# Performance work log

Measured on AMD Instinct MI355X. Metric: run time of the kernel, lower is better.

## Reference

```python
import jax, jax.numpy as jnp
import numpy as np

N = 50000        # nodes
E = 800000       # edges
IN_DIM, HID, OUT = 512, 256, 128
EPS = 1e-5       # PyG LayerNorm eps (added to std)


def setup_inputs() -> dict:
    key = jax.random.key(0)
    ks = jax.random.split(key, 24)
    def lin(k, i, o, scale=0.05):
        kw, kb = jax.random.split(k)
        return (jax.random.normal(kw, (i, o), jnp.float32) * scale,
                jax.random.normal(kb, (o,), jnp.float32) * scale)
    x = jax.random.normal(ks[0], (N, IN_DIM), jnp.float32)
    edge_index = jax.random.randint(ks[1], (2, E), 0, N, jnp.int64)
    Wq1, bq1 = lin(ks[2], IN_DIM, HID)
    Wk1, bk1 = lin(ks[3], IN_DIM, HID)
    Wv1, bv1 = lin(ks[4], IN_DIM, HID)
    Ws1, bs1 = lin(ks[5], IN_DIM, HID)
    g1 = jnp.ones((HID,), jnp.float32)
    be1 = jnp.zeros((HID,), jnp.float32)
    Wq2, bq2 = lin(ks[6], HID, OUT)
    Wk2, bk2 = lin(ks[7], HID, OUT)
    Wv2, bv2 = lin(ks[8], HID, OUT)
    Ws2, bs2 = lin(ks[9], HID, OUT)
    g2 = jnp.ones((OUT,), jnp.float32)
    be2 = jnp.zeros((OUT,), jnp.float32)
    return dict(x=x, Wq1=Wq1, bq1=bq1, Wk1=Wk1, bk1=bk1, Wv1=Wv1, bv1=bv1,
                Ws1=Ws1, bs1=bs1, g1=g1, be1=be1,
                Wq2=Wq2, bq2=bq2, Wk2=Wk2, bk2=bk2, Wv2=Wv2, bv2=bv2,
                Ws2=Ws2, bs2=bs2, g2=g2, be2=be2, edge_index=edge_index)


def transformer_conv(x, edge_index, Wq, bq, Wk, bk, Wv, bv, Ws, bs):
    # PyG TransformerConv, heads=1, concat=True, root_weight=True
    src, dst = edge_index[0], edge_index[1]
    n = x.shape[0]
    d = Wq.shape[1]
    q = x @ Wq + bq                               # [N, d]
    k = x @ Wk + bk
    v = x @ Wv + bv
    score = (q[dst] * k[src]).sum(-1) / jnp.sqrt(jnp.asarray(d, x.dtype))  # [E]
    m = jax.ops.segment_max(score, dst, num_segments=n)     # per-target max
    e = jnp.exp(score - m[dst])
    denom = jax.ops.segment_sum(e, dst, num_segments=n)
    alpha = e / denom[dst]                         # scatter-softmax over in-edges
    agg = jax.ops.segment_sum(alpha[:, None] * v[src], dst, num_segments=n)
    return agg + (x @ Ws + bs)                     # root/skip connection


def graph_layer_norm(h, w, b):
    # PyG LayerNorm mode='graph', no batch: normalize over ALL entries
    h = h - h.mean()
    return h / (h.std() + EPS) * w + b


def reference(x, Wq1, bq1, Wk1, bk1, Wv1, bv1, Ws1, bs1, g1, be1,
              Wq2, bq2, Wk2, bk2, Wv2, bv2, Ws2, bs2, g2, be2, edge_index):
    a1 = graph_layer_norm(
        transformer_conv(x, edge_index, Wq1, bq1, Wk1, bk1, Wv1, bv1, Ws1, bs1),
        g1, be1)
    h1 = jax.nn.elu(a1)  # ELU(alpha=1.0)
    h2 = graph_layer_norm(
        transformer_conv(h1, edge_index, Wq2, bq2, Wk2, bk2, Wv2, bv2, Ws2, bs2),
        g2, be2)
    return h2
```

## Files before the change

kernel.cpp:

```cpp
#include <hip/hip_runtime.h>
#include <stdint.h>
#include <math.h>

#define IN_DIM 512
#define HID    256
#define OUTD   128
#define LN_EPS 1e-5f
#define NSLOT  2048

typedef unsigned short u16;
typedef unsigned int   u32;
typedef short short8 __attribute__((ext_vector_type(8)));
typedef float f32x4  __attribute__((ext_vector_type(4)));

__device__ __forceinline__ float bf2f(u32 h) {
  union { u32 u; float f; } c; c.u = h << 16; return c.f;
}
__device__ __forceinline__ u16 f2bf(float f) {
  union { float f; u32 u; } c; c.f = f;
  u32 u = c.u;
  return (u16)((u + 0x7FFFu + ((u >> 16) & 1u)) >> 16);
}

__device__ __forceinline__ void gload_lds16(const void* g, void* l) {
  __builtin_amdgcn_global_load_lds((const __attribute__((address_space(1))) void*)g,
                                   (__attribute__((address_space(3))) void*)l, 16, 0, 0);
}

__global__ __launch_bounds__(256) void k_prep(
    const float* __restrict__ x, u16* __restrict__ x_bf, int n4,
    const int* __restrict__ edst, int* __restrict__ deg, int E,
    const float* __restrict__ bq1, const float* __restrict__ bk1,
    const float* __restrict__ bv1, const float* __restrict__ bs1,
    const float* __restrict__ bq2, const float* __restrict__ bk2,
    const float* __restrict__ bv2, const float* __restrict__ bs2,
    float* __restrict__ bc1, float* __restrict__ bc2,
    const float* __restrict__ Wq1, const float* __restrict__ Wk1,
    const float* __restrict__ Wv1, const float* __restrict__ Ws1,
    const float* __restrict__ Wq2, const float* __restrict__ Wk2,
    const float* __restrict__ Wv2, const float* __restrict__ Ws2,
    u16* __restrict__ Wt1, u16* __restrict__ Wt2,
    int b_cvt, int b_hist) {
  __shared__ u16 t[32][33];
  int blk = blockIdx.x;
  int tid = threadIdx.x;
  if (blk < b_cvt) {
    int id = blk * 256 + tid;
    if (id < n4) {
      const float4 v = ((const float4*)x)[id];
      ushort4 o;
      o.x = f2bf(v.x); o.y = f2bf(v.y); o.z = f2bf(v.z); o.w = f2bf(v.w);
      ((ushort4*)x_bf)[id] = o;
    }
    return;
  }
  blk -= b_cvt;
  if (blk < b_hist) {
    int e = blk * 256 + tid;
    if (e < E) atomicAdd(&deg[edst[e]], 1);
    return;
  }
  blk -= b_hist;
  if (blk < 6) {
    int id = blk * 256 + tid;
    if (id < 4 * HID) {
      const float* s = (id < HID) ? bq1 : (id < 2 * HID) ? bk1 : (id < 3 * HID) ? bv1 : bs1;
      bc1[id] = s[id & (HID - 1)];
    } else if (id < 4 * HID + 4 * OUTD) {
      int j = id - 4 * HID;
      const float* s = (j < OUTD) ? bq2 : (j < 2 * OUTD) ? bk2 : (j < 3 * OUTD) ? bv2 : bs2;
      bc2[j] = s[j & (OUTD - 1)];
    }
    return;
  }
  blk -= 6;
  int tx = tid & 31, ty = tid >> 5;
  if (blk < 512) {
    int mat = blk >> 7, r = blk & 127;
    int k0 = (r >> 3) * 32, n0 = (r & 7) * 32;
    const float* src = (mat == 0) ? Wq1 : (mat == 1) ? Wk1 : (mat == 2) ? Wv1 : Ws1;
    u16* dst = Wt1 + (size_t)mat * IN_DIM * HID;
#pragma unroll
    for (int i = 0; i < 32; i += 8)
      t[ty + i][tx] = f2bf(src[(size_t)(k0 + ty + i) * HID + n0 + tx]);
    __syncthreads();
#pragma unroll
    for (int i = 0; i < 32; i += 8)
      dst[(size_t)(n0 + ty + i) * IN_DIM + k0 + tx] = t[tx][ty + i];
    return;
  }
  blk -= 512;
  {
    int mat = blk >> 5, r = blk & 31;
    int k0 = (r >> 2) * 32, n0 = (r & 3) * 32;
    const float* src = (mat == 0) ? Wq2 : (mat == 1) ? Wk2 : (mat == 2) ? Wv2 : Ws2;
    u16* dst = Wt2 + (size_t)mat * HID * OUTD;
#pragma unroll
    for (int i = 0; i < 32; i += 8)
      t[ty + i][tx] = f2bf(src[(size_t)(k0 + ty + i) * OUTD + n0 + tx]);
    __syncthreads();
#pragma unroll
    for (int i = 0; i < 32; i += 8)
      dst[(size_t)(n0 + ty + i) * HID + k0 + tx] = t[tx][ty + i];
  }
}

__global__ __launch_bounds__(1024) void k_scan(const int* __restrict__ deg,
                                               int* __restrict__ offsets,
                                               int* __restrict__ cur, int n, int total) {
  __shared__ int sm[1024];
  int t = threadIdx.x;
  int chunk = (n + 1023) / 1024;
  int base = t * chunk;
  int s = 0;
  for (int i = base; i < base + chunk && i < n; ++i) s += deg[i];
  sm[t] = s;
  __syncthreads();
  for (int off = 1; off < 1024; off <<= 1) {
    int v = (t >= off) ? sm[t - off] : 0;
    __syncthreads();
    sm[t] += v;
    __syncthreads();
  }
  int run = sm[t] - s;
  for (int i = base; i < base + chunk && i < n; ++i) {
    offsets[i] = run;
    cur[i] = run;
    run += deg[i];
  }
  if (t == 0) offsets[n] = total;
}

__global__ void k_scatter(const int* __restrict__ src, const int* __restrict__ dst,
                          int* __restrict__ cursor, int* __restrict__ ssrc, int E) {
  int e = blockIdx.x * blockDim.x + threadIdx.x;
  if (e >= E) return;
  int d = dst[e];
  int pos = atomicAdd(&cursor[d], 1);
  ssrc[pos] = src[e];
}

__global__ __launch_bounds__(256) void k_gemm_bf16_nt(
    const u16* __restrict__ A, const u16* __restrict__ Bt, const float* __restrict__ bias,
    u16* __restrict__ C, int M, int K, int Nt) {
  __shared__ __align__(16) u16 As[128 * 32];
  __shared__ __align__(16) u16 Bs[128 * 32];
  const int tid = threadIdx.x;
  const int bm0 = blockIdx.x * 128;
  const int bn0 = blockIdx.y * 128;
  const int wave = tid >> 6, lane = tid & 63;
  const int q = lane >> 4, r16 = lane & 15;
  const int wm = (wave >> 1) * 64, wn = (wave & 1) * 64;

  f32x4 acc[4][4];
#pragma unroll
  for (int i = 0; i < 4; i++)
#pragma unroll
    for (int j = 0; j < 4; j++) acc[i][j] = (f32x4){0.f, 0.f, 0.f, 0.f};

  const int r0 = tid >> 2;
  const int c0 = (tid & 3) * 8;

  for (int kt = 0; kt < K; kt += 32) {
#pragma unroll
    for (int h = 0; h < 2; ++h) {
      int row = r0 + h * 64;
      gload_lds16(A + (size_t)(bm0 + row) * K + kt + c0, &As[row * 32 + c0]);
      gload_lds16(Bt + (size_t)(bn0 + row) * K + kt + c0, &Bs[row * 32 + c0]);
    }
    __syncthreads();
    short8 af[4], bfr[4];
#pragma unroll
    for (int i = 0; i < 4; i++) af[i] = *(const short8*)(&As[(wm + i * 16 + r16) * 32 + q * 8]);
#pragma unroll
    for (int j = 0; j < 4; j++) bfr[j] = *(const short8*)(&Bs[(wn + j * 16 + r16) * 32 + q * 8]);
#pragma unroll
    for (int i = 0; i < 4; i++)
#pragma unroll
      for (int j = 0; j < 4; j++)
        acc[i][j] = __builtin_amdgcn_mfma_f32_16x16x32_bf16(af[i], bfr[j], acc[i][j], 0, 0, 0);
    __syncthreads();
  }

#pragma unroll
  for (int i = 0; i < 4; i++) {
#pragma unroll
    for (int r = 0; r < 4; r++) {
      int grow = bm0 + wm + i * 16 + q * 4 + r;
      if (grow >= M) continue;
      size_t rbase = (size_t)grow * Nt;
#pragma unroll
      for (int j = 0; j < 4; j++) {
        int gcol = bn0 + wn + j * 16 + r16;
        float v = acc[i][j][r] + bias[gcol];
        C[rbase + gcol] = f2bf(v);
      }
    }
  }
}

template <int VPL>
__device__ __forceinline__ void load_bf(const u16* __restrict__ p, int lane, float* f) {
  if constexpr (VPL == 4) {
    uint2 r = *(const uint2*)(p + lane * 4);
    f[0] = bf2f(r.x & 0xffffu); f[1] = bf2f(r.x >> 16);
    f[2] = bf2f(r.y & 0xffffu); f[3] = bf2f(r.y >> 16);
  } else {
    u32 r = *(const u32*)(p + lane * 2);
    f[0] = bf2f(r & 0xffffu); f[1] = bf2f(r >> 16);
  }
}

template <int H, bool OUT_BF16>
__global__ __launch_bounds__(256) void k_conv(
    const u16* __restrict__ qkvs, const int* __restrict__ offsets,
    const int* __restrict__ ssrc, u16* __restrict__ out_bf,
    float* __restrict__ out_f, int n, float scale,
    float* __restrict__ ssum, float* __restrict__ ssq) {
  constexpr int VPL = H / 64;
  int gw = (blockIdx.x * blockDim.x + threadIdx.x) >> 6;
  int wave = threadIdx.x >> 6;
  int lane = threadIdx.x & 63;
  if (gw >= n) return;
  const u16* base = qkvs + (size_t)gw * (4 * H);
  float qf[VPL];
  load_bf<VPL>(base, lane, qf);
  int beg = offsets[gw], end = offsets[gw + 1];
  float m = -INFINITY, l = 0.f;
  float agg[VPL];
#pragma unroll
  for (int w = 0; w < VPL; w++) agg[w] = 0.f;

  int i = beg;
  for (; i + 4 <= end; i += 4) {
    int s0 = ssrc[i], s1 = ssrc[i + 1], s2 = ssrc[i + 2], s3 = ssrc[i + 3];
    const u16* k0p = qkvs + (size_t)s0 * (4 * H) + H;
    const u16* k1p = qkvs + (size_t)s1 * (4 * H) + H;
    const u16* k2p = qkvs + (size_t)s2 * (4 * H) + H;
    const u16* k3p = qkvs + (size_t)s3 * (4 * H) + H;
    float k0[VPL], k1[VPL], k2[VPL], k3[VPL];
    float v0[VPL], v1[VPL], v2[VPL], v3[VPL];
    load_bf<VPL>(k0p, lane, k0);
    load_bf<VPL>(k1p, lane, k1);
    load_bf<VPL>(k2p, lane, k2);
    load_bf<VPL>(k3p, lane, k3);
    load_bf<VPL>(k0p + H, lane, v0);
    load_bf<VPL>(k1p + H, lane, v1);
    load_bf<VPL>(k2p + H, lane, v2);
    load_bf<VPL>(k3p + H, lane, v3);
    float d0 = 0.f, d1 = 0.f, d2 = 0.f, d3 = 0.f;
#pragma unroll
    for (int w = 0; w < VPL; w++) {
      d0 += qf[w] * k0[w]; d1 += qf[w] * k1[w];
      d2 += qf[w] * k2[w]; d3 += qf[w] * k3[w];
    }
#pragma unroll
    for (int off = 32; off > 0; off >>= 1) {
      d0 += __shfl_xor(d0, off, 64);
      d1 += __shfl_xor(d1, off, 64);
      d2 += __shfl_xor(d2, off, 64);
      d3 += __shfl_xor(d3, off, 64);
    }
    d0 *= scale; d1 *= scale; d2 *= scale; d3 *= scale;
    float cm = fmaxf(fmaxf(d0, d1), fmaxf(d2, d3));
    float nm = fmaxf(m, cm);
    float sc = __expf(m - nm);
    float p0 = __expf(d0 - nm), p1 = __expf(d1 - nm);
    float p2 = __expf(d2 - nm), p3 = __expf(d3 - nm);
    m = nm;
    l = l * sc + (p0 + p1) + (p2 + p3);
#pragma unroll
    for (int w = 0; w < VPL; w++)
      agg[w] = agg[w] * sc + p0 * v0[w] + p1 * v1[w] + p2 * v2[w] + p3 * v3[w];
  }
  for (; i < end; ++i) {
    int s = ssrc[i];
    const u16* kb = qkvs + (size_t)s * (4 * H) + H;
    float kf[VPL], vf[VPL];
    load_bf<VPL>(kb, lane, kf);
    load_bf<VPL>(kb + H, lane, vf);
    float d = 0.f;
#pragma unroll
    for (int w = 0; w < VPL; w++) d += qf[w] * kf[w];
#pragma unroll
    for (int off = 32; off > 0; off >>= 1) d += __shfl_xor(d, off, 64);
    float score = d * scale;
    float nm = fmaxf(m, score);
    float sc = __expf(m - nm);
    float p = __expf(score - nm);
    m = nm;
    l = l * sc + p;
#pragma unroll
    for (int w = 0; w < VPL; w++) agg[w] = agg[w] * sc + p * vf[w];
  }

  float sf[VPL];
  load_bf<VPL>(base + 3 * H, lane, sf);
  float inv = (end > beg) ? 1.f / l : 0.f;
  float r[VPL];
#pragma unroll
  for (int w = 0; w < VPL; w++) {
    r[w] = agg[w] * inv + sf[w];
    if (OUT_BF16) out_bf[(size_t)gw * H + lane * VPL + w] = f2bf(r[w]);
    else out_f[(size_t)gw * H + lane * VPL + w] = r[w];
  }

  float s = 0.f, s2 = 0.f;
#pragma unroll
  for (int w = 0; w < VPL; w++) { s += r[w]; s2 += r[w] * r[w]; }
#pragma unroll
  for (int off = 32; off > 0; off >>= 1) {
    s += __shfl_xor(s, off, 64);
    s2 += __shfl_xor(s2, off, 64);
  }
  if (lane == 0) {
    int slot = (blockIdx.x * 4 + wave) & (NSLOT - 1);
    atomicAdd(&ssum[slot], s);
    atomicAdd(&ssq[slot], s2);
  }
}

__device__ __forceinline__ void slot_stats(const float* __restrict__ ssum,
                                           const float* __restrict__ ssq,
                                           double cnt, float& mu, float& inv) {
  __shared__ double rs[256], rq[256];
  double ls = 0.0, lq = 0.0;
  for (int i = threadIdx.x; i < NSLOT; i += 256) {
    ls += (double)ssum[i];
    lq += (double)ssq[i];
  }
  rs[threadIdx.x] = ls; rq[threadIdx.x] = lq;
  __syncthreads();
  for (int off = 128; off > 0; off >>= 1) {
    if (threadIdx.x < off) { rs[threadIdx.x] += rs[threadIdx.x + off]; rq[threadIdx.x] += rq[threadIdx.x + off]; }
    __syncthreads();
  }
  double mud = rs[0] / cnt;
  double var = rq[0] / cnt - mud * mud;
  if (var < 0.0) var = 0.0;
  mu = (float)mud;
  inv = (float)(1.0 / (sqrt(var) + (double)LN_EPS));
}

__global__ __launch_bounds__(256) void k_norm_elu_bf16(
    const u16* __restrict__ a, const float* __restrict__ g,
    const float* __restrict__ b, const float* __restrict__ ssum,
    const float* __restrict__ ssq, double cnt,
    u16* __restrict__ out, int n8, int Hmask) {
  float mu, inv;
  slot_stats(ssum, ssq, cnt, mu, inv);
  int id = blockIdx.x * blockDim.x + threadIdx.x;
  if (id >= n8) return;
  int i8 = id * 8;
  int cb = i8 & Hmask;
  uint4 v = *(const uint4*)(a + i8);
  const u32 va[4] = {v.x, v.y, v.z, v.w};
  uint4 o;
  u32* op = (u32*)&o;
#pragma unroll
  for (int w = 0; w < 4; w++) {
    float y0 = (bf2f(va[w] & 0xffffu) - mu) * inv * g[cb + 2 * w] + b[cb + 2 * w];
    float y1 = (bf2f(va[w] >> 16) - mu) * inv * g[cb + 2 * w + 1] + b[cb + 2 * w + 1];
    y0 = (y0 > 0.f) ? y0 : (__expf(y0) - 1.f);
    y1 = (y1 > 0.f) ? y1 : (__expf(y1) - 1.f);
    op[w] = (u32)f2bf(y0) | ((u32)f2bf(y1) << 16);
  }
  *(uint4*)(out + i8) = o;
}

__global__ __launch_bounds__(256) void k_norm_f32(
    float* __restrict__ a, const float* __restrict__ g,
    const float* __restrict__ b, const float* __restrict__ ssum,
    const float* __restrict__ ssq, double cnt, int n4, int Hmask) {
  float mu, inv;
  slot_stats(ssum, ssq, cnt, mu, inv);
  int id = blockIdx.x * blockDim.x + threadIdx.x;
  if (id >= n4) return;
  int i4 = id * 4;
  int cb = i4 & Hmask;
  float4 v = *(const float4*)(a + i4);
  float4 o;
  o.x = (v.x - mu) * inv * g[cb] + b[cb];
  o.y = (v.y - mu) * inv * g[cb + 1] + b[cb + 1];
  o.z = (v.z - mu) * inv * g[cb + 2] + b[cb + 2];
  o.w = (v.w - mu) * inv * g[cb + 3] + b[cb + 3];
  *(float4*)(a + i4) = o;
}

extern "C" void kernel_launch(void* const* d_in, const int* in_sizes, int n_in,
                              void* d_out, int out_size, void* d_ws, size_t ws_size,
                              hipStream_t stream) {
  const float* x   = (const float*)d_in[0];
  const float* Wq1 = (const float*)d_in[1];  const float* bq1 = (const float*)d_in[2];
  const float* Wk1 = (const float*)d_in[3];  const float* bk1 = (const float*)d_in[4];
  const float* Wv1 = (const float*)d_in[5];  const float* bv1 = (const float*)d_in[6];
  const float* Ws1 = (const float*)d_in[7];  const float* bs1 = (const float*)d_in[8];
  const float* g1  = (const float*)d_in[9];  const float* be1 = (const float*)d_in[10];
  const float* Wq2 = (const float*)d_in[11]; const float* bq2 = (const float*)d_in[12];
  const float* Wk2 = (const float*)d_in[13]; const float* bk2 = (const float*)d_in[14];
  const float* Wv2 = (const float*)d_in[15]; const float* bv2 = (const float*)d_in[16];
  const float* Ws2 = (const float*)d_in[17]; const float* bs2 = (const float*)d_in[18];
  const float* g2  = (const float*)d_in[19]; const float* be2 = (const float*)d_in[20];
  const int*   ei  = (const int*)d_in[21];

  const int N = in_sizes[0] / IN_DIM;
  const int E = in_sizes[21] / 2;
  const int* esrc = ei;
  const int* edst = ei + E;

  char* w = (char*)d_ws;
  auto carve = [&](size_t bytes) { char* p = w; w += (bytes + 255) & ~(size_t)255; return p; };
  int* deg     = (int*)carve((size_t)(N + 1) * 4);
  float* slots = (float*)carve(4 * NSLOT * 4);
  u16* x_bf  = (u16*)carve((size_t)N * IN_DIM * 2);
  u16* Wt1   = (u16*)carve((size_t)4 * HID * IN_DIM * 2);
  u16* Wt2   = (u16*)carve((size_t)4 * OUTD * HID * 2);
  float* bc1 = (float*)carve(4 * HID * 4);
  float* bc2 = (float*)carve(4 * OUTD * 4);
  u16* qkvs1 = (u16*)carve((size_t)N * 4 * HID * 2);
  u16* a1    = (u16*)carve((size_t)N * HID * 2);
  int* offs  = (int*)carve((size_t)(N + 1) * 4);
  int* cur   = (int*)carve((size_t)(N + 1) * 4);
  int* ssrc  = (int*)carve((size_t)E * 4);
  u16* h1    = x_bf;
  u16* qkvs2 = qkvs1;
  float* ssum1 = slots, *ssq1 = slots + NSLOT;
  float* ssum2 = slots + 2 * NSLOT, *ssq2 = slots + 3 * NSLOT;

  hipMemsetAsync(deg, 0, (size_t)((char*)(slots + 4 * NSLOT) - (char*)deg), stream);

  int n4 = N * IN_DIM / 4;
  int b_cvt = (n4 + 255) / 256;
  int b_hist = (E + 255) / 256;
  int k1_blocks = b_cvt + b_hist + 6 + 512 + 128;
  k_prep<<<k1_blocks, 256, 0, stream>>>(
      x, x_bf, n4, edst, deg, E,
      bq1, bk1, bv1, bs1, bq2, bk2, bv2, bs2, bc1, bc2,
      Wq1, Wk1, Wv1, Ws1, Wq2, Wk2, Wv2, Ws2, Wt1, Wt2, b_cvt, b_hist);

  k_scan<<<1, 1024, 0, stream>>>(deg, offs, cur, N, E);

  k_scatter<<<b_hist, 256, 0, stream>>>(esrc, edst, cur, ssrc, E);

  dim3 gg1((N + 127) / 128, (4 * HID) / 128);
  k_gemm_bf16_nt<<<gg1, 256, 0, stream>>>(x_bf, Wt1, bc1, qkvs1, N, IN_DIM, 4 * HID);

  k_conv<HID, true><<<(N + 3) / 4, 256, 0, stream>>>(qkvs1, offs, ssrc, a1, nullptr, N,
                                                     1.0f / sqrtf((float)HID), ssum1, ssq1);
  k_norm_elu_bf16<<<N * HID / 8 / 256, 256, 0, stream>>>(
      a1, g1, be1, ssum1, ssq1, (double)N * HID, h1, N * HID / 8, HID - 1);

  dim3 gg2((N + 127) / 128, (4 * OUTD) / 128);
  k_gemm_bf16_nt<<<gg2, 256, 0, stream>>>(h1, Wt2, bc2, qkvs2, N, HID, 4 * OUTD);

  k_conv<OUTD, false><<<(N + 3) / 4, 256, 0, stream>>>(qkvs2, offs, ssrc, nullptr, (float*)d_out,
                                                       N, 1.0f / sqrtf((float)OUTD), ssum2, ssq2);
  k_norm_f32<<<N * OUTD / 4 / 256, 256, 0, stream>>>(
      (float*)d_out, g2, be2, ssum2, ssq2, (double)N * OUTD, N * OUTD / 4, OUTD - 1);
}
```

Measured before the change: 740.4 us.

## Parallelize degree prefix scan and widen GEMM tile to 128x256

Replaces the single-block 1024-thread serial-chunk scan of node degrees with a three-kernel parallel scan: per-block sums, a scan of the block sums, and a final per-block scan. Separately widens the bf16 MFMA GEMM tile from 128x128 to 128x256, so each wave holds 4x8 accumulators and A tiles are reused across twice as many columns, halving the grid's y dimension. The scan change removes a serialized single-workgroup bottleneck at the cost of two extra launches. The GEMM change raises register pressure and LDS usage and cuts block count, which can hurt occupancy.

```diff
diff --git a/kernel.cpp b/kernel.cpp
--- a/kernel.cpp
+++ b/kernel.cpp
@@ -105,30 +105,54 @@
   }
 }
 
-__global__ __launch_bounds__(1024) void k_scan(const int* __restrict__ deg,
-                                               int* __restrict__ offsets,
-                                               int* __restrict__ cur, int n, int total) {
-  __shared__ int sm[1024];
+__global__ void k_block_sum(const int* __restrict__ deg, int* __restrict__ bsum, int n) {
+  __shared__ int sm[256];
+  int i = blockIdx.x * 256 + threadIdx.x;
+  sm[threadIdx.x] = (i < n) ? deg[i] : 0;
+  __syncthreads();
+  for (int off = 128; off > 0; off >>= 1) {
+    if (threadIdx.x < off) sm[threadIdx.x] += sm[threadIdx.x + off];
+    __syncthreads();
+  }
+  if (threadIdx.x == 0) bsum[blockIdx.x] = sm[0];
+}
+
+__global__ void k_scan_bsum(const int* __restrict__ bsum, int* __restrict__ boff, int nb) {
+  __shared__ int sm[256];
   int t = threadIdx.x;
-  int chunk = (n + 1023) / 1024;
-  int base = t * chunk;
-  int s = 0;
-  for (int i = base; i < base + chunk && i < n; ++i) s += deg[i];
-  sm[t] = s;
+  int v = (t < nb) ? bsum[t] : 0;
+  sm[t] = v;
   __syncthreads();
-  for (int off = 1; off < 1024; off <<= 1) {
-    int v = (t >= off) ? sm[t - off] : 0;
-    __syncthreads();
-    sm[t] += v;
-    __syncthreads();
-  }
-  int run = sm[t] - s;
-  for (int i = base; i < base + chunk && i < n; ++i) {
-    offsets[i] = run;
-    cur[i] = run;
-    run += deg[i];
-  }
-  if (t == 0) offsets[n] = total;
+  for (int off = 1; off < 256; off <<= 1) {
+    int tmp = (t >= off) ? sm[t - off] : 0;
+    __syncthreads();
+    sm[t] += tmp;
+    __syncthreads();
+  }
+  if (t < nb) boff[t] = sm[t] - v;
+}
+
+__global__ void k_scan_final(const int* __restrict__ deg, const int* __restrict__ boff,
+                             int* __restrict__ offsets, int* __restrict__ cur,
+                             int n, int total) {
+  __shared__ int sm[256];
+  int t = threadIdx.x;
+  int i = blockIdx.x * 256 + t;
+  int v = (i < n) ? deg[i] : 0;
+  sm[t] = v;
+  __syncthreads();
+  for (int off = 1; off < 256; off <<= 1) {
+    int tmp = (t >= off) ? sm[t - off] : 0;
+    __syncthreads();
+    sm[t] += tmp;
+    __syncthreads();
+  }
+  if (i < n) {
+    int o = boff[blockIdx.x] + sm[t] - v;
+    offsets[i] = o;
+    cur[i] = o;
+  }
+  if (i == 0) offsets[n] = total;
 }
 
 __global__ void k_scatter(const int* __restrict__ src, const int* __restrict__ dst,
@@ -140,45 +164,48 @@
   ssrc[pos] = src[e];
 }
 
-__global__ __launch_bounds__(256) void k_gemm_bf16_nt(
+__global__ __launch_bounds__(256, 2) void k_gemm_bf16_nt(
     const u16* __restrict__ A, const u16* __restrict__ Bt, const float* __restrict__ bias,
     u16* __restrict__ C, int M, int K, int Nt) {
   __shared__ __align__(16) u16 As[128 * 32];
-  __shared__ __align__(16) u16 Bs[128 * 32];
+  __shared__ __align__(16) u16 Bs[256 * 32];
   const int tid = threadIdx.x;
   const int bm0 = blockIdx.x * 128;
-  const int bn0 = blockIdx.y * 128;
+  const int bn0 = blockIdx.y * 256;
   const int wave = tid >> 6, lane = tid & 63;
   const int q = lane >> 4, r16 = lane & 15;
-  const int wm = (wave >> 1) * 64, wn = (wave & 1) * 64;
-
-  f32x4 acc[4][4];
+  const int wm = (wave >> 1) * 64;
+  const int wn = (wave & 1) * 128;
+
+  f32x4 acc[4][8];
 #pragma unroll
   for (int i = 0; i < 4; i++)
 #pragma unroll
-    for (int j = 0; j < 4; j++) acc[i][j] = (f32x4){0.f, 0.f, 0.f, 0.f};
-
-  const int r0 = tid >> 2;
-  const int c0 = (tid & 3) * 8;
+    for (int j = 0; j < 8; j++) acc[i][j] = (f32x4){0.f, 0.f, 0.f, 0.f};
 
   for (int kt = 0; kt < K; kt += 32) {
 #pragma unroll
-    for (int h = 0; h < 2; ++h) {
-      int row = r0 + h * 64;
-      gload_lds16(A + (size_t)(bm0 + row) * K + kt + c0, &As[row * 32 + c0]);
-      gload_lds16(Bt + (size_t)(bn0 + row) * K + kt + c0, &Bs[row * 32 + c0]);
-    }
-    __syncthreads();
-    short8 af[4], bfr[4];
-#pragma unroll
-    for (int i = 0; i < 4; i++) af[i] = *(const short8*)(&As[(wm + i * 16 + r16) * 32 + q * 8]);
-#pragma unroll
-    for (int j = 0; j < 4; j++) bfr[j] = *(const short8*)(&Bs[(wn + j * 16 + r16) * 32 + q * 8]);
-#pragma unroll
-    for (int i = 0; i < 4; i++)
-#pragma unroll
-      for (int j = 0; j < 4; j++)
-        acc[i][j] = __builtin_amdgcn_mfma_f32_16x16x32_bf16(af[i], bfr[j], acc[i][j], 0, 0, 0);
+    for (int j = 0; j < 2; ++j) {
+      int t = j * 256 + tid;
+      gload_lds16(A + (size_t)(bm0 + (t >> 2)) * K + kt + (t & 3) * 8, &As[t * 8]);
+    }
+#pragma unroll
+    for (int j = 0; j < 4; ++j) {
+      int t = j * 256 + tid;
+      gload_lds16(Bt + (size_t)(bn0 + (t >> 2)) * K + kt + (t & 3) * 8, &Bs[t * 8]);
+    }
+    __syncthreads();
+    short8 bfr[8];
+#pragma unroll
+    for (int j = 0; j < 8; ++j)
+      bfr[j] = *(const short8*)(&Bs[(wn + j * 16 + r16) * 32 + q * 8]);
+#pragma unroll
+    for (int i = 0; i < 4; ++i) {
+      short8 af = *(const short8*)(&As[(wm + i * 16 + r16) * 32 + q * 8]);
+#pragma unroll
+      for (int j = 0; j < 8; ++j)
+        acc[i][j] = __builtin_amdgcn_mfma_f32_16x16x32_bf16(af, bfr[j], acc[i][j], 0, 0, 0);
+    }
     __syncthreads();
   }
 
@@ -190,7 +217,7 @@
       if (grow >= M) continue;
       size_t rbase = (size_t)grow * Nt;
 #pragma unroll
-      for (int j = 0; j < 4; j++) {
+      for (int j = 0; j < 8; j++) {
         int gcol = bn0 + wn + j * 16 + r16;
         float v = acc[i][j][r] + bias[gcol];
         C[rbase + gcol] = f2bf(v);
@@ -422,6 +449,8 @@
   int* offs  = (int*)carve((size_t)(N + 1) * 4);
   int* cur   = (int*)carve((size_t)(N + 1) * 4);
   int* ssrc  = (int*)carve((size_t)E * 4);
+  int* bsum  = (int*)carve(1024);
+  int* boff  = (int*)carve(1024);
   u16* h1    = x_bf;
   u16* qkvs2 = qkvs1;
   float* ssum1 = slots, *ssq1 = slots + NSLOT;
@@ -438,11 +467,14 @@
       bq1, bk1, bv1, bs1, bq2, bk2, bv2, bs2, bc1, bc2,
       Wq1, Wk1, Wv1, Ws1, Wq2, Wk2, Wv2, Ws2, Wt1, Wt2, b_cvt, b_hist);
 
-  k_scan<<<1, 1024, 0, stream>>>(deg, offs, cur, N, E);
+  int nb = (N + 255) / 256;
+  k_block_sum<<<nb, 256, 0, stream>>>(deg, bsum, N);
+  k_scan_bsum<<<1, 256, 0, stream>>>(bsum, boff, nb);
+  k_scan_final<<<nb, 256, 0, stream>>>(deg, boff, offs, cur, N, E);
 
   k_scatter<<<b_hist, 256, 0, stream>>>(esrc, edst, cur, ssrc, E);
 
-  dim3 gg1((N + 127) / 128, (4 * HID) / 128);
+  dim3 gg1((N + 127) / 128, (4 * HID) / 256);
   k_gemm_bf16_nt<<<gg1, 256, 0, stream>>>(x_bf, Wt1, bc1, qkvs1, N, IN_DIM, 4 * HID);
 
   k_conv<HID, true><<<(N + 3) / 4, 256, 0, stream>>>(qkvs1, offs, ssrc, a1, nullptr, N,
@@ -450,7 +482,7 @@
   k_norm_elu_bf16<<<N * HID / 8 / 256, 256, 0, stream>>>(
       a1, g1, be1, ssum1, ssq1, (double)N * HID, h1, N * HID / 8, HID - 1);
 
-  dim3 gg2((N + 127) / 128, (4 * OUTD) / 128);
+  dim3 gg2((N + 127) / 128, (4 * OUTD) / 256);
   k_gemm_bf16_nt<<<gg2, 256, 0, stream>>>(h1, Wt2, bc2, qkvs2, N, HID, 4 * OUTD);
 
   k_conv<OUTD, false><<<(N + 3) / 4, 256, 0, stream>>>(qkvs2, offs, ssrc, nullptr, (float*)d_out,
```

After: 622.9 us. -15.9%, faster.
